# Kernel tuning notes

Measured on AMD Instinct MI355X. Metric: run time of the kernel, lower is better.

Reference implementation:

```python
import jax, jax.numpy as jnp
import numpy as np

N_NODES = 100000
IN_CH = 128
HID = 128
OUT_CH = 40
K = 3
N_EDGES = 3200000


def setup_inputs() -> dict:
    key = jax.random.key(0)
    ks = jax.random.split(key, 10)
    x = jax.random.normal(ks[0], (N_NODES, IN_CH), dtype=jnp.float32)
    edge_index = jax.random.randint(ks[1], (2, N_EDGES), 0, N_NODES, dtype=jnp.int64)
    s1 = 1.0 / np.sqrt(IN_CH)
    lin1_w = jax.random.uniform(ks[2], (IN_CH, HID), minval=-s1, maxval=s1, dtype=jnp.float32)
    lin1_b = jax.random.uniform(ks[3], (HID,), minval=-s1, maxval=s1, dtype=jnp.float32)
    s2 = 1.0 / np.sqrt(HID)
    gcn_w = jax.random.uniform(ks[4], (K, HID, HID), minval=-s2, maxval=s2, dtype=jnp.float32)
    gcn_b = jnp.zeros((K, HID), dtype=jnp.float32)
    lin2_w = jax.random.uniform(ks[5], (HID, OUT_CH), minval=-s2, maxval=s2, dtype=jnp.float32)
    lin2_b = jax.random.uniform(ks[6], (OUT_CH,), minval=-s2, maxval=s2, dtype=jnp.float32)
    return {"x": x, "edge_index": edge_index, "lin1_w": lin1_w, "lin1_b": lin1_b,
            "gcn_w": gcn_w, "gcn_b": gcn_b, "lin2_w": lin2_w, "lin2_b": lin2_b}


def _gcn_conv(h, w, b, src, dst, norm, n):
    # PyG GCNConv: transform, then symmetric-normalized aggregation (self-loops
    # already included in src/dst/norm), then bias.
    h = h @ w  # [N, H]
    msg = h[src] * norm[:, None]  # [E+N, H] gathered edge messages
    out = jax.ops.segment_sum(msg, dst, num_segments=n)
    return out + b


def reference(x, edge_index, lin1_w, lin1_b, gcn_w, gcn_b, lin2_w, lin2_b):
    n = x.shape[0]
    src, dst = edge_index[0], edge_index[1]
    # add self-loops (GCNConv default add_self_loops=True)
    loop = jnp.arange(n, dtype=src.dtype)
    src = jnp.concatenate([src, loop])
    dst = jnp.concatenate([dst, loop])
    # symmetric normalization D^{-1/2} (A+I) D^{-1/2}
    deg = jax.ops.segment_sum(jnp.ones(src.shape[0], dtype=x.dtype), dst, num_segments=n)
    dinv = jnp.where(deg > 0, jax.lax.rsqrt(deg), 0.0)
    norm = dinv[src] * dinv[dst]  # [E+N]

    h = jax.nn.relu(x @ lin1_w + lin1_b)  # dropout: eval mode (identity)
    for k in range(K):
        h = jax.nn.relu(_gcn_conv(h, gcn_w[k], gcn_b[k], src, dst, norm, n))
    logits = h @ lin2_w + lin2_b
    return jax.nn.log_softmax(logits, axis=1)
```

## Files before the change

### kernel.cpp

```cpp
#include <hip/hip_runtime.h>
#include <math.h>

#define NN 100000
#define NP 100032
#define HIDC 128
#define OUTC 40
#define NBUCK ((NN + 511) >> 9)
#define PT_TILE 4096
#define BCAP 18368
#define NRG 8
#define RG_SHIFT 14

typedef __attribute__((ext_vector_type(2))) float floatx2;
typedef __attribute__((ext_vector_type(4))) float floatx4;
typedef __attribute__((ext_vector_type(8))) short short8;
typedef __attribute__((ext_vector_type(4))) unsigned uintx4;

__device__ __forceinline__ unsigned pack_bf16x2(float a, float b) {
  unsigned ua = __float_as_uint(a), ub = __float_as_uint(b);
  ua = ua + 0x7fff + ((ua >> 16) & 1);
  ub = ub + 0x7fff + ((ub >> 16) & 1);
  return (ua >> 16) | (ub & 0xffff0000u);
}
__device__ __forceinline__ unsigned short bf16r(float x) {
  unsigned u = __float_as_uint(x);
  u = u + 0x7fff + ((u >> 16) & 1);
  return (unsigned short)(u >> 16);
}


__global__ __launch_bounds__(512) void partition_kernel(
    const int* __restrict__ src, const int* __restrict__ dst,
    int* __restrict__ bcur, unsigned* __restrict__ pairs, int E) {
  __shared__ int hist[256];
  __shared__ int lcur[256];
  __shared__ int startl[256];
  __shared__ int gofs[256];
  __shared__ unsigned lbuf[PT_TILE];
  int t = threadIdx.x;
  if (t < 256) { hist[t] = 0; lcur[t] = 0; }
  __syncthreads();
  int e0 = blockIdx.x * PT_TILE;
  int ec = E - e0; if (ec > PT_TILE) ec = PT_TILE;

  int dr[8], sr[8];
#pragma unroll
  for (int k = 0; k < 8; k++) {
    int i = t + (k << 9);
    if (i < ec) {
      int d = dst[e0 + i];
      dr[k] = d; sr[k] = src[e0 + i];
      atomicAdd(&hist[d >> 9], 1);
    }
  }
  __syncthreads();

  int h = (t < 256) ? hist[t] : 0;
  if (t < 256) startl[t] = h;
  __syncthreads();
  for (int off = 1; off < 256; off <<= 1) {
    int u = (t < 256 && t >= off) ? startl[t - off] : 0;
    __syncthreads();
    if (t < 256) startl[t] += u;
    __syncthreads();
  }
  if (t < 256) {
    int st = startl[t] - h;
    int gb = (h > 0) ? atomicAdd(&bcur[t], h) : 0;
    gofs[t] = gb - st;
    startl[t] = st;
  }
  __syncthreads();

#pragma unroll
  for (int k = 0; k < 8; k++) {
    int i = t + (k << 9);
    if (i < ec) {
      int d = dr[k];
      int b = d >> 9;
      int q = atomicAdd(&lcur[b], 1);
      lbuf[startl[b] + q] = ((unsigned)(d & 511) << 17) | (unsigned)sr[k];
    }
  }
  __syncthreads();

  for (int pos = t; pos < ec; pos += 512) {
    int lo = 0, hi = 255;
    while (lo < hi) {
      int mid = (lo + hi + 1) >> 1;
      if (startl[mid] <= pos) lo = mid; else hi = mid - 1;
    }
    pairs[gofs[lo] + pos] = lbuf[pos];
  }
}

__global__ __launch_bounds__(1024) void bucket_fill_kernel(
    const unsigned* __restrict__ pairs, const int* __restrict__ bcur,
    float* __restrict__ dinv, int* __restrict__ csr,
    int* __restrict__ sbeg, int* __restrict__ send,
    float* __restrict__ sdinv, int* __restrict__ sdn, int N) {
  int b = blockIdx.x;
  int d0 = b << 9;
  int nd = N - d0; if (nd > 512) nd = 512;
  __shared__ int hist8[512 * NRG];
  __shared__ int cur8[512 * NRG];
  __shared__ int sums[512];
  __shared__ int dh[256];
  int t = threadIdx.x;
#pragma unroll
  for (int k = 0; k < NRG / 2; k++) hist8[t + k * 1024] = 0;
  __syncthreads();
  int rbeg = b * BCAP, rend = bcur[b];
  for (int i = rbeg + t; i < rend; i += 1024) {
    unsigned pk = pairs[i];
    atomicAdd(&hist8[(int)(pk >> 17) * NRG + (int)((pk & 0x1FFFF) >> RG_SHIFT)], 1);
  }
  __syncthreads();
  int h = 0;
  int hr[NRG];
  if (t < 512) {
#pragma unroll
    for (int r = 0; r < NRG; r++) { hr[r] = hist8[t * NRG + r]; h += hr[r]; }
    sums[t] = h;
  }
  __syncthreads();
  for (int off = 1; off < 512; off <<= 1) {
    int u = (t < 512 && t >= off) ? sums[t - off] : 0;
    __syncthreads();
    if (t < 512) sums[t] += u;
    __syncthreads();
  }
  int base = 0; float di = 0.f;
  if (t < 512) {
    base = rbeg + sums[t] - h;
    di = rsqrtf((float)(h + 1));
    int a = base;
#pragma unroll
    for (int r = 0; r < NRG; r++) { cur8[t * NRG + r] = a; a += hr[r]; }
    if (t < nd) dinv[d0 + t] = di;
  }
  __syncthreads();

  if (t < 128) dh[t] = 0;
  __syncthreads();
  int c = h < 127 ? h : 127;
  if (t < nd) atomicAdd(&dh[c], 1);
  __syncthreads();
  int dv = (t < 128) ? dh[t] : 0;
  if (t < 128) sums[t] = dv;
  __syncthreads();
  for (int off = 1; off < 128; off <<= 1) {
    int u = (t < 128 && t >= off) ? sums[t - off] : 0;
    __syncthreads();
    if (t < 128) sums[t] += u;
    __syncthreads();
  }
  if (t < 128) dh[128 + t] = sums[t] - dv;
  __syncthreads();
  if (t < nd) {
    int pos = d0 + atomicAdd(&dh[128 + c], 1);
    sbeg[pos] = base; send[pos] = base + h; sdinv[pos] = di; sdn[pos] = d0 + t;
  }
  __syncthreads();

  for (int i = rbeg + t; i < rend; i += 1024) {
    unsigned pk = pairs[i];
    int srcv = (int)(pk & 0x1FFFF);
    int q = atomicAdd(&cur8[(int)(pk >> 17) * NRG + (srcv >> RG_SHIFT)], 1);
    csr[q] = srcv;
  }
}


__global__ __launch_bounds__(256) void prep_misc_kernel(
    const float* __restrict__ lin1_w, const float* __restrict__ gcn_w,
    const float* __restrict__ lin2_w, int* __restrict__ bcur,
    unsigned short* __restrict__ Wt, unsigned short* __restrict__ W2t) {
  int b = blockIdx.x;
  int t = threadIdx.x;
  if (b == 0) {
    if (t < NBUCK) bcur[t] = t * BCAP;
  } else if (b <= 32) {
    int m = (b - 1) >> 3;
    int chunk = (b - 1) & 7;
    const float* src = (m == 0) ? lin1_w : (gcn_w + (size_t)(m - 1) * 16384);
    unsigned short* dstp = Wt + (size_t)m * 16384;
    int i0 = chunk * 2048;
    for (int i = i0 + t; i < i0 + 2048; i += 256) {
      int n = i >> 7, k = i & 127;
      dstp[(size_t)n * 128 + k] = bf16r(src[(size_t)k * 128 + n]);
    }
  } else {
    int chunk = b - 33;
    int i0 = chunk * 3072;
    for (int i = i0 + t; i < i0 + 3072; i += 256) {
      int n = i >> 7, k = i & 127;
      W2t[i] = (n < OUTC) ? bf16r(lin2_w[(size_t)k * OUTC + n]) : (unsigned short)0;
    }
  }
}


template <int MODE>
__global__ __launch_bounds__(256) void gemm_mfma_kernel(
    const void* __restrict__ Av, const unsigned short* __restrict__ Wt,
    const float* __restrict__ bias, const float* __restrict__ dinv,
    void* __restrict__ Y, int M) {
  int t = threadIdx.x;
  int w = t >> 6;
  int l = t & 63;
  int quad = l >> 4;
  int m16 = l & 15;
  int row0 = blockIdx.x * 64;
  int colbase = w * 32;

  floatx4 acc[4][2];
#pragma unroll
  for (int rt = 0; rt < 4; rt++)
#pragma unroll
    for (int ct = 0; ct < 2; ct++) acc[rt][ct] = (floatx4)0.f;

#pragma unroll
  for (int kc = 0; kc < 4; kc++) {
    int kof = kc * 32 + quad * 8;
    short8 a0 = *(const short8*)(Wt + (size_t)(colbase + m16) * 128 + kof);
    short8 a1 = *(const short8*)(Wt + (size_t)(colbase + 16 + m16) * 128 + kof);
#pragma unroll
    for (int rt = 0; rt < 4; rt++) {
      short8 bfr;
      if (MODE == 2) {
        const float* Af = (const float*)Av + (size_t)(row0 + rt * 16 + m16) * 128 + kof;
        float4 f0 = *(const float4*)Af;
        float4 f1 = *(const float4*)(Af + 4);
        unsigned u0 = pack_bf16x2(f0.x, f0.y);
        unsigned u1 = pack_bf16x2(f0.z, f0.w);
        unsigned u2 = pack_bf16x2(f1.x, f1.y);
        unsigned u3 = pack_bf16x2(f1.z, f1.w);
        bfr[0] = (short)(u0 & 0xFFFF); bfr[1] = (short)(u0 >> 16);
        bfr[2] = (short)(u1 & 0xFFFF); bfr[3] = (short)(u1 >> 16);
        bfr[4] = (short)(u2 & 0xFFFF); bfr[5] = (short)(u2 >> 16);
        bfr[6] = (short)(u3 & 0xFFFF); bfr[7] = (short)(u3 >> 16);
      } else {
        bfr = *(const short8*)((const unsigned short*)Av +
                               (size_t)(row0 + rt * 16 + m16) * 128 + kof);
      }
      acc[rt][0] = __builtin_amdgcn_mfma_f32_16x16x32_bf16(a0, bfr, acc[rt][0], 0, 0, 0);
      acc[rt][1] = __builtin_amdgcn_mfma_f32_16x16x32_bf16(a1, bfr, acc[rt][1], 0, 0, 0);
    }
  }

  if (MODE != 1) {
    unsigned short* Y16 = (unsigned short*)Y;
    float4 bv0 = *(const float4*)(bias + colbase + quad * 4);
    float4 bv1 = *(const float4*)(bias + colbase + 16 + quad * 4);
#pragma unroll
    for (int rt = 0; rt < 4; rt++) {
      int row = row0 + rt * 16 + m16;
      if (row < M) {
        uint2 s0, s1;
        s0.x = pack_bf16x2(fmaxf(acc[rt][0][0] + bv0.x, 0.f),
                           fmaxf(acc[rt][0][1] + bv0.y, 0.f));
        s0.y = pack_bf16x2(fmaxf(acc[rt][0][2] + bv0.z, 0.f),
                           fmaxf(acc[rt][0][3] + bv0.w, 0.f));
        s1.x = pack_bf16x2(fmaxf(acc[rt][1][0] + bv1.x, 0.f),
                           fmaxf(acc[rt][1][1] + bv1.y, 0.f));
        s1.y = pack_bf16x2(fmaxf(acc[rt][1][2] + bv1.z, 0.f),
                           fmaxf(acc[rt][1][3] + bv1.w, 0.f));
        *(uint2*)(Y16 + (size_t)row * 128 + colbase + quad * 4) = s0;
        *(uint2*)(Y16 + (size_t)row * 128 + colbase + 16 + quad * 4) = s1;
      }
    }
  } else {
    unsigned* Y8 = (unsigned*)Y;
#pragma unroll
    for (int rt = 0; rt < 4; rt++) {
      int row = row0 + rt * 16 + m16;
      if (row < M) {
        float dd = dinv[row];
        unsigned u0 = 0, u1 = 0;
        u0 = __builtin_amdgcn_cvt_pk_fp8_f32(acc[rt][0][0] * dd, acc[rt][0][1] * dd, (int)u0, false);
        u0 = __builtin_amdgcn_cvt_pk_fp8_f32(acc[rt][0][2] * dd, acc[rt][0][3] * dd, (int)u0, true);
        u1 = __builtin_amdgcn_cvt_pk_fp8_f32(acc[rt][1][0] * dd, acc[rt][1][1] * dd, (int)u1, false);
        u1 = __builtin_amdgcn_cvt_pk_fp8_f32(acc[rt][1][2] * dd, acc[rt][1][3] * dd, (int)u1, true);
        Y8[(size_t)row * 32 + (colbase >> 2) + quad] = u0;
        Y8[(size_t)row * 32 + ((colbase + 16) >> 2) + quad] = u1;
      }
    }
  }
}


#define ACC8(u)                                                       \
  acc[0] += __builtin_amdgcn_cvt_pk_f32_fp8((int)(u).x, false);       \
  acc[1] += __builtin_amdgcn_cvt_pk_f32_fp8((int)(u).x, true);        \
  acc[2] += __builtin_amdgcn_cvt_pk_f32_fp8((int)(u).y, false);       \
  acc[3] += __builtin_amdgcn_cvt_pk_f32_fp8((int)(u).y, true);        \
  acc[4] += __builtin_amdgcn_cvt_pk_f32_fp8((int)(u).z, false);       \
  acc[5] += __builtin_amdgcn_cvt_pk_f32_fp8((int)(u).z, true);        \
  acc[6] += __builtin_amdgcn_cvt_pk_f32_fp8((int)(u).w, false);       \
  acc[7] += __builtin_amdgcn_cvt_pk_f32_fp8((int)(u).w, true);

__global__ __launch_bounds__(256) void aggregate_fp8_kernel(
    const uint4* __restrict__ Ht8, const int* __restrict__ csr,
    const int* __restrict__ sbeg, const int* __restrict__ send,
    const float* __restrict__ sdinv, const int* __restrict__ sdn,
    const float* __restrict__ bias, uint4* __restrict__ Out, int N) {
  int wid = (blockIdx.x * blockDim.x + threadIdx.x) >> 6;
  int lane = threadIdx.x & 63;
  int g = lane >> 3;
  int c8 = lane & 7;
  int bucket = wid % NBUCK;
  int band = wid / NBUCK;
  int idx = (bucket << 9) + (band << 3) + g;
  if (idx >= N) return;
  int beg = sbeg[idx], end = send[idx];
  int d = sdn[idx];

  floatx2 acc[8];
  {
    uint4 us = Ht8[(size_t)d * 8 + c8];
    acc[0] = __builtin_amdgcn_cvt_pk_f32_fp8((int)us.x, false);
    acc[1] = __builtin_amdgcn_cvt_pk_f32_fp8((int)us.x, true);
    acc[2] = __builtin_amdgcn_cvt_pk_f32_fp8((int)us.y, false);
    acc[3] = __builtin_amdgcn_cvt_pk_f32_fp8((int)us.y, true);
    acc[4] = __builtin_amdgcn_cvt_pk_f32_fp8((int)us.z, false);
    acc[5] = __builtin_amdgcn_cvt_pk_f32_fp8((int)us.z, true);
    acc[6] = __builtin_amdgcn_cvt_pk_f32_fp8((int)us.w, false);
    acc[7] = __builtin_amdgcn_cvt_pk_f32_fp8((int)us.w, true);
  }
  int i = beg;
  int s0, s1, s2, s3, s4, s5, s6, s7;
  if (i + 7 < end) {
    s0 = csr[i];     s1 = csr[i + 1]; s2 = csr[i + 2]; s3 = csr[i + 3];
    s4 = csr[i + 4]; s5 = csr[i + 5]; s6 = csr[i + 6]; s7 = csr[i + 7];
  }
  while (i + 7 < end) {
    uint4 u0 = Ht8[(size_t)s0 * 8 + c8];
    uint4 u1 = Ht8[(size_t)s1 * 8 + c8];
    uint4 u2 = Ht8[(size_t)s2 * 8 + c8];
    uint4 u3 = Ht8[(size_t)s3 * 8 + c8];
    uint4 u4 = Ht8[(size_t)s4 * 8 + c8];
    uint4 u5 = Ht8[(size_t)s5 * 8 + c8];
    uint4 u6 = Ht8[(size_t)s6 * 8 + c8];
    uint4 u7 = Ht8[(size_t)s7 * 8 + c8];
    i += 8;
    if (i + 7 < end) {
      s0 = csr[i];     s1 = csr[i + 1]; s2 = csr[i + 2]; s3 = csr[i + 3];
      s4 = csr[i + 4]; s5 = csr[i + 5]; s6 = csr[i + 6]; s7 = csr[i + 7];
    }
    ACC8(u0) ACC8(u1) ACC8(u2) ACC8(u3) ACC8(u4) ACC8(u5) ACC8(u6) ACC8(u7)
  }
  if (i + 3 < end) {
    int t0 = csr[i], t1 = csr[i + 1], t2 = csr[i + 2], t3 = csr[i + 3];
    uint4 u0 = Ht8[(size_t)t0 * 8 + c8];
    uint4 u1 = Ht8[(size_t)t1 * 8 + c8];
    uint4 u2 = Ht8[(size_t)t2 * 8 + c8];
    uint4 u3 = Ht8[(size_t)t3 * 8 + c8];
    ACC8(u0) ACC8(u1) ACC8(u2) ACC8(u3)
    i += 4;
  }
  for (; i < end; ++i) {
    uint4 u0 = Ht8[(size_t)csr[i] * 8 + c8];
    ACC8(u0)
  }

  float dd = sdinv[idx];
  const float4* b4 = (const float4*)bias;
  float4 bv0 = b4[4 * c8 + 0];
  float4 bv1 = b4[4 * c8 + 1];
  float4 bv2 = b4[4 * c8 + 2];
  float4 bv3 = b4[4 * c8 + 3];
  uintx4 o0, o1;
  o0.x = pack_bf16x2(fmaxf(fmaf(dd, acc[0][0], bv0.x), 0.f),
                     fmaxf(fmaf(dd, acc[0][1], bv0.y), 0.f));
  o0.y = pack_bf16x2(fmaxf(fmaf(dd, acc[1][0], bv0.z), 0.f),
                     fmaxf(fmaf(dd, acc[1][1], bv0.w), 0.f));
  o0.z = pack_bf16x2(fmaxf(fmaf(dd, acc[2][0], bv1.x), 0.f),
                     fmaxf(fmaf(dd, acc[2][1], bv1.y), 0.f));
  o0.w = pack_bf16x2(fmaxf(fmaf(dd, acc[3][0], bv1.z), 0.f),
                     fmaxf(fmaf(dd, acc[3][1], bv1.w), 0.f));
  o1.x = pack_bf16x2(fmaxf(fmaf(dd, acc[4][0], bv2.x), 0.f),
                     fmaxf(fmaf(dd, acc[4][1], bv2.y), 0.f));
  o1.y = pack_bf16x2(fmaxf(fmaf(dd, acc[5][0], bv2.z), 0.f),
                     fmaxf(fmaf(dd, acc[5][1], bv2.w), 0.f));
  o1.z = pack_bf16x2(fmaxf(fmaf(dd, acc[6][0], bv3.x), 0.f),
                     fmaxf(fmaf(dd, acc[6][1], bv3.y), 0.f));
  o1.w = pack_bf16x2(fmaxf(fmaf(dd, acc[7][0], bv3.z), 0.f),
                     fmaxf(fmaf(dd, acc[7][1], bv3.w), 0.f));
  __builtin_nontemporal_store(o0, (uintx4*)(Out + (size_t)d * 16 + 2 * c8));
  __builtin_nontemporal_store(o1, (uintx4*)(Out + (size_t)d * 16 + 2 * c8 + 1));
}


__global__ __launch_bounds__(256) void head_mfma_kernel(
    const unsigned short* __restrict__ A, const unsigned short* __restrict__ W2t,
    const float* __restrict__ b2, float* __restrict__ Out, int N) {
  __shared__ float lg[64][48];
  __shared__ float bs[48];
  int t = threadIdx.x;
  int w = t >> 6, l = t & 63, quad = l >> 4, m16 = l & 15;
  if (t < 48) bs[t] = (t < OUTC) ? b2[t] : 0.f;
  int row0 = blockIdx.x * 64;

  floatx4 acc[3];
  acc[0] = (floatx4)0.f; acc[1] = (floatx4)0.f; acc[2] = (floatx4)0.f;
  const unsigned short* Aw = A + (size_t)(row0 + w * 16) * 128;
#pragma unroll
  for (int kc = 0; kc < 4; kc++) {
    int kof = kc * 32 + quad * 8;
    short8 a = *(const short8*)(Aw + (size_t)m16 * 128 + kof);
#pragma unroll
    for (int ct = 0; ct < 3; ct++) {
      short8 b = *(const short8*)(W2t + (size_t)(ct * 16 + m16) * 128 + kof);
      acc[ct] = __builtin_amdgcn_mfma_f32_16x16x32_bf16(a, b, acc[ct], 0, 0, 0);
    }
  }
#pragma unroll
  for (int ct = 0; ct < 3; ct++)
#pragma unroll
    for (int j = 0; j < 4; j++)
      lg[w * 16 + quad * 4 + j][ct * 16 + m16] = acc[ct][j];
  __syncthreads();

  int r = t >> 2, sub = t & 3;
  int row = row0 + r;
  float vals[10];
  float mx = -3.4e38f;
#pragma unroll
  for (int j = 0; j < 10; j++) {
    float v = lg[r][sub * 10 + j] + bs[sub * 10 + j];
    vals[j] = v;
    mx = fmaxf(mx, v);
  }
  mx = fmaxf(mx, __shfl_xor(mx, 1, 64));
  mx = fmaxf(mx, __shfl_xor(mx, 2, 64));
  float se = 0.f;
#pragma unroll
  for (int j = 0; j < 10; j++) se += expf(vals[j] - mx);
  se += __shfl_xor(se, 1, 64);
  se += __shfl_xor(se, 2, 64);
  if (row < N) {
    float ls = logf(se);
#pragma unroll
    for (int j = 0; j < 10; j++)
      Out[(size_t)row * OUTC + sub * 10 + j] = vals[j] - mx - ls;
  }
}


extern "C" void kernel_launch(void* const* d_in, const int* in_sizes, int n_in,
                              void* d_out, int out_size, void* d_ws, size_t ws_size,
                              hipStream_t stream) {
  const float* x      = (const float*)d_in[0];
  const int*   edge   = (const int*)d_in[1];
  const float* lin1_w = (const float*)d_in[2];
  const float* lin1_b = (const float*)d_in[3];
  const float* gcn_w  = (const float*)d_in[4];
  const float* gcn_b  = (const float*)d_in[5];
  const float* lin2_w = (const float*)d_in[6];
  const float* lin2_b = (const float*)d_in[7];
  float* out = (float*)d_out;

  const int N = NN;
  const int E = in_sizes[1] / 2;
  const int* src = edge;
  const int* dst = edge + E;

  char* p = (char*)d_ws;
  auto alloc = [&](size_t bytes) { char* q = p; p += (bytes + 255) & ~(size_t)255; return q; };
  unsigned*       hA16    = (unsigned*)alloc((size_t)NP * 128 * 2);
  unsigned*       hB8     = (unsigned*)alloc((size_t)NP * 32 * 4);
  unsigned*       pairs   = (unsigned*)alloc((size_t)NBUCK * BCAP * 4);
  int*            csr     = (int*)alloc((size_t)NBUCK * BCAP * 4);
  float*          dinv    = (float*)alloc((size_t)NP * 4);
  int*            sbeg    = (int*)alloc((size_t)N * 4);
  int*            send    = (int*)alloc((size_t)N * 4);
  float*          sdinv   = (float*)alloc((size_t)N * 4);
  int*            sdn     = (int*)alloc((size_t)N * 4);
  unsigned short* Wt      = (unsigned short*)alloc((size_t)4 * 16384 * 2);
  unsigned short* W2t     = (unsigned short*)alloc((size_t)48 * 128 * 2);
  int*            bcur    = (int*)alloc(256 * 4);

  prep_misc_kernel<<<35, 256, 0, stream>>>(lin1_w, gcn_w, lin2_w, bcur, Wt, W2t);
  partition_kernel<<<(E + PT_TILE - 1) / PT_TILE, 512, 0, stream>>>(src, dst, bcur, pairs, E);
  bucket_fill_kernel<<<NBUCK, 1024, 0, stream>>>(pairs, bcur, dinv, csr,
                                                 sbeg, send, sdinv, sdn, N);

  int gb = NP / 64;
  gemm_mfma_kernel<2><<<gb, 256, 0, stream>>>((const void*)x, Wt,
                                              lin1_b, nullptr, (void*)hA16, N);
  int ablocks = (NBUCK * 64) / 4;
  for (int k = 0; k < 3; k++) {
    gemm_mfma_kernel<1><<<gb, 256, 0, stream>>>((const void*)hA16,
                                                Wt + (size_t)(k + 1) * 16384,
                                                nullptr, dinv, (void*)hB8, N);
    aggregate_fp8_kernel<<<ablocks, 256, 0, stream>>>(
        (const uint4*)hB8, csr, sbeg, send, sdinv, sdn, gcn_b + (size_t)k * 128,
        (uint4*)hA16, N);
  }
  head_mfma_kernel<<<gb, 256, 0, stream>>>((const unsigned short*)hA16, W2t,
                                           lin2_b, out, N);
}
```

Measured before the change: 470.6 us.

## Stage bucket pairs in LDS and write CSR coalesced; double partition tile

The bucket fill kernel now loads each bucket's packed pairs into shared memory once, so the second pass rereads LDS instead of global memory. Instead of scattering CSR writes to global memory through atomics, it builds a local permutation in LDS and then writes the CSR range in order with coalesced stores. Separately, the partition kernel tile grows from 4096 to 8192 edges per block, which halves the number of global bucket-cursor atomics. The cost is about 110 KB of extra LDS per block in the fill kernel, which limits occupancy, and more registers per thread in the partition kernel.

```diff
diff --git a/kernel.cpp b/kernel.cpp
--- a/kernel.cpp
+++ b/kernel.cpp
@@ -6,7 +6,7 @@
 #define HIDC 128
 #define OUTC 40
 #define NBUCK ((NN + 511) >> 9)
-#define PT_TILE 4096
+#define PT_TILE 8192
 #define BCAP 18368
 #define NRG 8
 #define RG_SHIFT 14
@@ -43,9 +43,9 @@
   int e0 = blockIdx.x * PT_TILE;
   int ec = E - e0; if (ec > PT_TILE) ec = PT_TILE;
 
-  int dr[8], sr[8];
-#pragma unroll
-  for (int k = 0; k < 8; k++) {
+  int dr[16], sr[16];
+#pragma unroll
+  for (int k = 0; k < 16; k++) {
     int i = t + (k << 9);
     if (i < ec) {
       int d = dst[e0 + i];
@@ -73,7 +73,7 @@
   __syncthreads();
 
 #pragma unroll
-  for (int k = 0; k < 8; k++) {
+  for (int k = 0; k < 16; k++) {
     int i = t + (k << 9);
     if (i < ec) {
       int d = dr[k];
@@ -102,6 +102,8 @@
   int b = blockIdx.x;
   int d0 = b << 9;
   int nd = N - d0; if (nd > 512) nd = 512;
+  __shared__ unsigned lbuf[BCAP];
+  __shared__ unsigned short perm[BCAP];
   __shared__ int hist8[512 * NRG];
   __shared__ int cur8[512 * NRG];
   __shared__ int sums[512];
@@ -109,10 +111,12 @@
   int t = threadIdx.x;
 #pragma unroll
   for (int k = 0; k < NRG / 2; k++) hist8[t + k * 1024] = 0;
-  __syncthreads();
-  int rbeg = b * BCAP, rend = bcur[b];
-  for (int i = rbeg + t; i < rend; i += 1024) {
-    unsigned pk = pairs[i];
+  int rbeg = b * BCAP;
+  int cnt = bcur[b] - rbeg;
+  for (int i = t; i < cnt; i += 1024) lbuf[i] = pairs[rbeg + i];
+  __syncthreads();
+  for (int i = t; i < cnt; i += 1024) {
+    unsigned pk = lbuf[i];
     atomicAdd(&hist8[(int)(pk >> 17) * NRG + (int)((pk & 0x1FFFF) >> RG_SHIFT)], 1);
   }
   __syncthreads();
@@ -130,11 +134,11 @@
     if (t < 512) sums[t] += u;
     __syncthreads();
   }
-  int base = 0; float di = 0.f;
+  int lbase = 0; float di = 0.f;
   if (t < 512) {
-    base = rbeg + sums[t] - h;
+    lbase = sums[t] - h;
     di = rsqrtf((float)(h + 1));
-    int a = base;
+    int a = lbase;
 #pragma unroll
     for (int r = 0; r < NRG; r++) { cur8[t * NRG + r] = a; a += hr[r]; }
     if (t < nd) dinv[d0 + t] = di;
@@ -159,16 +163,20 @@
   __syncthreads();
   if (t < nd) {
     int pos = d0 + atomicAdd(&dh[128 + c], 1);
-    sbeg[pos] = base; send[pos] = base + h; sdinv[pos] = di; sdn[pos] = d0 + t;
-  }
-  __syncthreads();
-
-  for (int i = rbeg + t; i < rend; i += 1024) {
-    unsigned pk = pairs[i];
-    int srcv = (int)(pk & 0x1FFFF);
-    int q = atomicAdd(&cur8[(int)(pk >> 17) * NRG + (srcv >> RG_SHIFT)], 1);
-    csr[q] = srcv;
-  }
+    sbeg[pos] = rbeg + lbase; send[pos] = rbeg + lbase + h;
+    sdinv[pos] = di; sdn[pos] = d0 + t;
+  }
+  __syncthreads();
+
+  for (int i = t; i < cnt; i += 1024) {
+    unsigned pk = lbuf[i];
+    int q = atomicAdd(&cur8[(int)(pk >> 17) * NRG + (int)((pk & 0x1FFFF) >> RG_SHIFT)], 1);
+    perm[q] = (unsigned short)i;
+  }
+  __syncthreads();
+
+  for (int pos = t; pos < cnt; pos += 1024)
+    csr[rbeg + pos] = (int)(lbuf[perm[pos]] & 0x1FFFF);
 }
 
 
```

After: 454.8 us. -3.3%, faster.
